# Performance work log

Hardware: AMD Instinct MI355X
Metric: run time of the kernel (lower is better)

Reference implementation:

```python
import jax, jax.numpy as jnp
import numpy as np


def _deform_unfold(feat, offset):
    """Deformable 3x3 unfold with bilinear sampling, zero padding outside.
    feat: [B,C,H,W], offset: [B,2K,H,W] (y,x per point). Returns [B,C,K,H,W]."""
    B, C, H, W = feat.shape
    K = offset.shape[1] // 2
    off = offset.reshape(B, K, 2, H, W)
    # 3x3 kernel grid, dilation 1, padding 1 -> relative taps in {-1,0,1}
    ky = (jnp.arange(K) // 3 - 1).astype(feat.dtype)
    kx = (jnp.arange(K) % 3 - 1).astype(feat.dtype)
    hh = jnp.arange(H, dtype=feat.dtype)
    ww = jnp.arange(W, dtype=feat.dtype)
    py = hh[None, None, :, None] + ky[None, :, None, None] + off[:, :, 0]  # [B,K,H,W]
    px = ww[None, None, None, :] + kx[None, :, None, None] + off[:, :, 1]  # [B,K,H,W]
    y0 = jnp.floor(py)
    x0 = jnp.floor(px)
    fy = py - y0  # frac weights
    fx = px - x0
    y0i = y0.astype(jnp.int32)
    x0i = x0.astype(jnp.int32)

    def gather(yi, xi):
        valid = ((yi >= 0) & (yi < H) & (xi >= 0) & (xi < W)).astype(feat.dtype)
        yc = jnp.clip(yi, 0, H - 1)
        xc = jnp.clip(xi, 0, W - 1)
        v = jax.vmap(lambda f, yy, xx: f[:, yy, xx])(feat, yc, xc)  # [B,C,K,H,W]
        return v * valid[:, None]

    w00 = ((1 - fy) * (1 - fx))[:, None]
    w01 = ((1 - fy) * fx)[:, None]
    w10 = (fy * (1 - fx))[:, None]
    w11 = (fy * fx)[:, None]
    return (gather(y0i, x0i) * w00 + gather(y0i, x0i + 1) * w01 +
            gather(y0i + 1, x0i) * w10 + gather(y0i + 1, x0i + 1) * w11)


def setup_inputs() -> dict:
    key = jax.random.key(0)
    ks = jax.random.split(key, 8)
    B, C, H, W = 4, 256, 64, 64
    Ci, P = 128, 9
    x = jax.random.normal(ks[0], (B, C, H, W), jnp.float32)
    offset = jax.random.normal(ks[1], (B, 2 * P, H, W), jnp.float32)
    std = 0.01  # normal_init(std=0.01)
    Wq = jax.random.normal(ks[2], (Ci, C), jnp.float32) * std
    Wk = jax.random.normal(ks[3], (Ci, C), jnp.float32) * std
    Wv = jax.random.normal(ks[4], (Ci, C), jnp.float32) * std
    Wo = jax.random.normal(ks[5], (Ci,), jnp.float32) * std
    bq = jnp.zeros((Ci,), jnp.float32)
    bk = jnp.zeros((Ci,), jnp.float32)
    bv = jnp.zeros((Ci,), jnp.float32)
    bo = jnp.zeros((1,), jnp.float32)
    return {"x": x, "offset": offset, "Wq": Wq, "bq": bq, "Wk": Wk, "bk": bk,
            "Wv": Wv, "bv": bv, "Wo": Wo, "bo": bo}


def reference(x, offset, Wq, bq, Wk, bk, Wv, bv, Wo, bo):
    # 1x1 conv projections
    q = jnp.einsum('bchw,oc->bohw', x, Wq) + bq[None, :, None, None]
    k = jnp.einsum('bchw,oc->bohw', x, Wk) + bk[None, :, None, None]
    v = jnp.einsum('bchw,oc->bohw', x, Wv) + bv[None, :, None, None]
    qu = _deform_unfold(q, offset)  # [B,Ci,K,H,W]
    ku = _deform_unfold(k, offset)  # [B,Ci,K,H,W]
    vu = _deform_unfold(v, offset)  # [B,Ci,K,H,W]
    # per-pixel KxK attention: query [K,Ci] @ key [Ci,K]
    scores = jnp.einsum('bcihw,bcjhw->bijhw', qu, ku)  # [B,K,K,H,W]
    attn = jax.nn.softmax(scores, axis=2)
    # attn [K,K] @ value [K,Ci]
    out_v = jnp.einsum('bijhw,bcjhw->bcihw', attn, vu)  # [B,Ci,K,H,W]
    # conv_out: 1x1 conv Ci->1 over the value, then sigmoid -> [B,K,H,W]
    out = jnp.einsum('bcihw,c->bihw', out_v, Wo) + bo[0]
    return jax.nn.sigmoid(out)
```

## Files before the change

kernel.cpp:

```cpp
#include <hip/hip_runtime.h>

typedef unsigned short u16;
typedef unsigned int u32;

#define B_   4
#define C_   256
#define CI_  128
#define H_   64
#define W_   64
#define NPB_ 4096
#define NP_  16384
#define K_   9
#define MROWS_ 272

typedef __attribute__((ext_vector_type(8))) __bf16 bf16x8_t;
typedef __attribute__((ext_vector_type(4))) float f32x4_t;
typedef __attribute__((ext_vector_type(2))) float f32x2_t;

__device__ __forceinline__ float bf2f(u16 u) {
    union { u32 i; float f; } x; x.i = ((u32)u) << 16; return x.f;
}
__device__ __forceinline__ float bf2f_lo(u32 w) {
    union { u32 i; float f; } x; x.i = w << 16; return x.f;
}
__device__ __forceinline__ float bf2f_hi(u32 w) {
    union { u32 i; float f; } x; x.i = w & 0xffff0000u; return x.f;
}
__device__ __forceinline__ u16 f2bf(float f) {
    union { float f; u32 i; } x; x.f = f;
    u32 lsb = (x.i >> 16) & 1u;
    return (u16)((x.i + 0x7fffu + lsb) >> 16);
}
__device__ __forceinline__ void acc8p(f32x2_t* f, uint4 v, f32x2_t w2) {
    f32x2_t p;
    p.x = bf2f_lo(v.x); p.y = bf2f_hi(v.x); f[0] += w2 * p;
    p.x = bf2f_lo(v.y); p.y = bf2f_hi(v.y); f[1] += w2 * p;
    p.x = bf2f_lo(v.z); p.y = bf2f_hi(v.z); f[2] += w2 * p;
    p.x = bf2f_lo(v.w); p.y = bf2f_hi(v.w); f[3] += w2 * p;
}

__global__ void k0b_prep(const float* __restrict__ Wq, const float* __restrict__ bq,
                         const float* __restrict__ Wk, const float* __restrict__ bk,
                         const float* __restrict__ Wv, const float* __restrict__ bv,
                         const float* __restrict__ Wo,
                         u16* __restrict__ Wt, float* __restrict__ bias) {
    const int o = blockIdx.x;
    const int c = threadIdx.x;
    u16 val;
    if (o < 128) {
        val = f2bf(Wq[o * C_ + c]);
        if (c == 0) bias[o] = bq[o];
    } else if (o < 256) {
        val = f2bf(Wk[(o - 128) * C_ + c]);
        if (c == 0) bias[o] = bk[o - 128];
    } else if (o == 256) {
        float s = 0.f;
        #pragma unroll 8
        for (int oo = 0; oo < CI_; ++oo)
            s += Wo[oo] * Wv[oo * C_ + c];
        val = f2bf(s);
        if (c == 0) {
            float ts = 0.f;
            #pragma unroll 8
            for (int oo = 0; oo < CI_; ++oo) ts += Wo[oo] * bv[oo];
            bias[256] = ts;
        }
    } else {
        val = 0;
        if (c == 0) bias[o] = 0.f;
    }
    const int mt = o >> 4, l16 = o & 15;
    const int kk = c >> 5, g = (c >> 3) & 3, e = c & 7;
    Wt[(size_t)((mt * 8 + kk) * 64 + g * 16 + l16) * 8 + e] = val;
}

__global__ __launch_bounds__(512) void k1_proj(
    const float* __restrict__ x, const u16* __restrict__ Wt,
    const float* __restrict__ bias,
    u16* __restrict__ qk, float* __restrict__ vs) {
    __shared__ u16 xs[16][272];
    const int t = threadIdx.x;
    const int l = t & 63;
    const int w = t >> 6;
    const int lane16 = l & 15;
    const int g = l >> 4;
    const int p0 = blockIdx.x * 16;
    const int b = p0 >> 12;
    const int pin = p0 & 4095;

    {
        const int spx = t & 15, cg = t >> 4;
        const float* src = x + (size_t)(b * C_ + cg * 8) * NPB_ + pin + spx;
        float v[8];
        #pragma unroll
        for (int i = 0; i < 8; ++i) v[i] = src[(size_t)i * NPB_];
        uint4 pk;
        pk.x = (u32)f2bf(v[0]) | ((u32)f2bf(v[1]) << 16);
        pk.y = (u32)f2bf(v[2]) | ((u32)f2bf(v[3]) << 16);
        pk.z = (u32)f2bf(v[4]) | ((u32)f2bf(v[5]) << 16);
        pk.w = (u32)f2bf(v[6]) | ((u32)f2bf(v[7]) << 16);
        *reinterpret_cast<uint4*>(&xs[spx][cg * 8]) = pk;
    }
    __syncthreads();

    const int mts[3] = {2 * w, 2 * w + 1, 16};
    f32x4_t acc[3];
    #pragma unroll
    for (int n = 0; n < 3; ++n)
        #pragma unroll
        for (int r = 0; r < 4; ++r)
            acc[n][r] = bias[mts[n] * 16 + g * 4 + r];

    #pragma unroll
    for (int kk = 0; kk < 8; ++kk) {
        const bf16x8_t bv = *reinterpret_cast<const bf16x8_t*>(&xs[lane16][kk * 32 + g * 8]);
        #pragma unroll
        for (int n = 0; n < 3; ++n) {
            const bf16x8_t av = *reinterpret_cast<const bf16x8_t*>(
                Wt + (size_t)((mts[n] * 8 + kk) * 64 + l) * 8);
            acc[n] = __builtin_amdgcn_mfma_f32_16x16x32_bf16(av, bv, acc[n], 0, 0, 0);
        }
    }

    const int px = p0 + lane16;
    u16* qrow = qk + (size_t)px * C_;
    #pragma unroll
    for (int n = 0; n < 2; ++n) {
        const int mt = mts[n];
        u32* dst = reinterpret_cast<u32*>(qrow + mt * 16 + g * 4);
        dst[0] = (u32)f2bf(acc[n][0]) | ((u32)f2bf(acc[n][1]) << 16);
        dst[1] = (u32)f2bf(acc[n][2]) | ((u32)f2bf(acc[n][3]) << 16);
    }
    if (w == 0 && g == 0) vs[px] = acc[2][0];
}

__global__ __launch_bounds__(256, 1) void k2_attn(
    const float* __restrict__ off, const u16* __restrict__ qk,
    const float* __restrict__ vs, const float* __restrict__ bo,
    float* __restrict__ out) {
    const int t = threadIdx.x;
    const int l = t & 63;
    const int bid = blockIdx.x;
    const int swz = (bid & 7) * ((int)gridDim.x >> 3) + (bid >> 3);
    const int pixel = swz * 4 + (t >> 6);
    const int b = pixel >> 12;
    const int rem = pixel & 4095;
    const int y = rem >> 6, xx = rem & 63;
    const int l16 = l & 15;
    const int tap = (l16 < K_) ? l16 : (K_ - 1);
    const int g = l >> 4;

    const float* offb = off + ((size_t)b * (2 * K_) + 2 * tap) * NPB_ + rem;
    const float oy = offb[0];
    const float ox = offb[NPB_];
    const float py = (float)(y + tap / 3 - 1) + oy;
    const float px = (float)(xx + tap % 3 - 1) + ox;
    const float fy0 = floorf(py), fx0 = floorf(px);
    const float fy = py - fy0, fx = px - fx0;
    const int y0 = (int)fy0, x0 = (int)fx0;

    const u16* qkb = qk + ((size_t)(b << 12)) * C_ + g * 8;
    const float* vsm = vs + (b << 12);

    float wgt[4];
    int ppc[4];
    const u16* bp[4];
    #pragma unroll
    for (int c = 0; c < 4; ++c) {
        const int dy = c >> 1, dx = c & 1;
        const int yi = y0 + dy, xi = x0 + dx;
        const float wv = (dy ? fy : 1.f - fy) * (dx ? fx : 1.f - fx);
        const int ok = (yi >= 0) & (yi < H_) & (xi >= 0) & (xi < W_);
        const int yc = min(max(yi, 0), H_ - 1);
        const int xc = min(max(xi, 0), W_ - 1);
        ppc[c] = yc * W_ + xc;
        wgt[c] = ok ? wv : 0.f;
        bp[c] = qkb + (size_t)ppc[c] * C_;
    }

    uint4 qv[4][4], kv[4][4];
    #pragma unroll
    for (int c = 0; c < 4; ++c) {
        #pragma unroll
        for (int s = 0; s < 4; ++s) {
            qv[c][s] = *reinterpret_cast<const uint4*>(bp[c] + s * 32);
            kv[c][s] = *reinterpret_cast<const uint4*>(bp[c] + CI_ + s * 32);
        }
    }
    float vsc[4];
    #pragma unroll
    for (int c = 0; c < 4; ++c) vsc[c] = vsm[ppc[c]];
    __builtin_amdgcn_sched_barrier(0);

    const float vsu_t = wgt[0] * vsc[0] + wgt[1] * vsc[1] +
                        wgt[2] * vsc[2] + wgt[3] * vsc[3];

    f32x2_t fq[16], fk[16];
    #pragma unroll
    for (int e = 0; e < 16; ++e) { fq[e] = (f32x2_t){0.f, 0.f}; fk[e] = (f32x2_t){0.f, 0.f}; }
    #pragma unroll
    for (int s = 0; s < 4; ++s) {
        #pragma unroll
        for (int c = 0; c < 4; ++c) {
            const f32x2_t w2 = {wgt[c], wgt[c]};
            acc8p(&fq[s * 4], qv[c][s], w2);
            acc8p(&fk[s * 4], kv[c][s], w2);
        }
    }

    f32x4_t acc = {0.f, 0.f, 0.f, 0.f};
    #pragma unroll
    for (int s = 0; s < 4; ++s) {
        bf16x8_t av, bv;
        #pragma unroll
        for (int e = 0; e < 4; ++e) {
            av[2 * e]     = (__bf16)fk[s * 4 + e].x;
            av[2 * e + 1] = (__bf16)fk[s * 4 + e].y;
            bv[2 * e]     = (__bf16)fq[s * 4 + e].x;
            bv[2 * e + 1] = (__bf16)fq[s * 4 + e].y;
        }
        acc = __builtin_amdgcn_mfma_f32_16x16x32_bf16(av, bv, acc, 0, 0, 0);
    }

    float mx = -1e30f;
    #pragma unroll
    for (int r = 0; r < 4; ++r) {
        const int j = g * 4 + r;
        if (j < K_) mx = fmaxf(mx, acc[r]);
    }
    mx = fmaxf(mx, __shfl_xor(mx, 16, 64));
    mx = fmaxf(mx, __shfl_xor(mx, 32, 64));

    float vj[4];
    #pragma unroll
    for (int r = 0; r < 4; ++r) vj[r] = __shfl(vsu_t, g * 4 + r, 64);

    float den = 0.f, num = 0.f;
    #pragma unroll
    for (int r = 0; r < 4; ++r) {
        const int j = g * 4 + r;
        if (j < K_) {
            const float e = __expf(acc[r] - mx);
            den += e;
            num += e * vj[r];
        }
    }
    den += __shfl_xor(den, 16, 64); den += __shfl_xor(den, 32, 64);
    num += __shfl_xor(num, 16, 64); num += __shfl_xor(num, 32, 64);

    if (l < K_) {
        const float z = num / den + bo[0];
        out[(size_t)b * K_ * NPB_ + (size_t)l * NPB_ + rem] = 1.f / (1.f + __expf(-z));
    }
}

extern "C" void kernel_launch(void* const* d_in, const int* in_sizes, int n_in,
                              void* d_out, int out_size, void* d_ws, size_t ws_size,
                              hipStream_t stream) {
    const float* x   = (const float*)d_in[0];
    const float* off = (const float*)d_in[1];
    const float* Wq  = (const float*)d_in[2];
    const float* bq  = (const float*)d_in[3];
    const float* Wk  = (const float*)d_in[4];
    const float* bk  = (const float*)d_in[5];
    const float* Wv  = (const float*)d_in[6];
    const float* bv  = (const float*)d_in[7];
    const float* Wo  = (const float*)d_in[8];
    const float* bo  = (const float*)d_in[9];
    float* out = (float*)d_out;

    char* ws = (char*)d_ws;
    u16*   qkbuf = (u16*)(ws + 4096);
    float* vsmap = (float*)(ws + 4096 + 8388608);
    u16*   Wt    = (u16*)(ws + 4096 + 8388608 + 65536);
    float* bias  = (float*)(ws + 4096 + 8388608 + 65536 + 139264);

    k0b_prep<<<MROWS_, 256, 0, stream>>>(Wq, bq, Wk, bk, Wv, bv, Wo, Wt, bias);
    k1_proj<<<NP_ / 16, 512, 0, stream>>>(x, Wt, bias, qkbuf, vsmap);
    k2_attn<<<NP_ / 4, 256, 0, stream>>>(off, qkbuf, vsmap, bo, out);
}
```

Before: 76.93 us.

## Compute attention on raw corner rows via MFMA, apply bilinear weights afterwards

The attention kernel no longer interpolates q/k rows in fp32 and then repacks them to bf16. Each lane now loads one bilinear corner row for up to three taps and feeds the raw bf16 rows straight into a 3x3 grid of MFMAs. The bilinear weights are applied to the 16x16 corner-pair score tiles afterwards using shuffles. This removes the conversion and FMA work and the large register footprint, and the 1-wave-per-SIMD launch bound is dropped to allow higher occupancy. In exchange it issues nine times as many MFMAs plus many cross-lane shuffles, and rounding differs because q/k are no longer re-quantised after interpolation.

Result: no change. 77.93 us (median of 2 runs) (+1.3%).

```diff
diff --git a/kernel.cpp b/kernel.cpp
--- a/kernel.cpp
+++ b/kernel.cpp
@@ -15,28 +15,11 @@
 
 typedef __attribute__((ext_vector_type(8))) __bf16 bf16x8_t;
 typedef __attribute__((ext_vector_type(4))) float f32x4_t;
-typedef __attribute__((ext_vector_type(2))) float f32x2_t;
-
-__device__ __forceinline__ float bf2f(u16 u) {
-    union { u32 i; float f; } x; x.i = ((u32)u) << 16; return x.f;
-}
-__device__ __forceinline__ float bf2f_lo(u32 w) {
-    union { u32 i; float f; } x; x.i = w << 16; return x.f;
-}
-__device__ __forceinline__ float bf2f_hi(u32 w) {
-    union { u32 i; float f; } x; x.i = w & 0xffff0000u; return x.f;
-}
+
 __device__ __forceinline__ u16 f2bf(float f) {
     union { float f; u32 i; } x; x.f = f;
     u32 lsb = (x.i >> 16) & 1u;
     return (u16)((x.i + 0x7fffu + lsb) >> 16);
-}
-__device__ __forceinline__ void acc8p(f32x2_t* f, uint4 v, f32x2_t w2) {
-    f32x2_t p;
-    p.x = bf2f_lo(v.x); p.y = bf2f_hi(v.x); f[0] += w2 * p;
-    p.x = bf2f_lo(v.y); p.y = bf2f_hi(v.y); f[1] += w2 * p;
-    p.x = bf2f_lo(v.z); p.y = bf2f_hi(v.z); f[2] += w2 * p;
-    p.x = bf2f_lo(v.w); p.y = bf2f_hi(v.w); f[3] += w2 * p;
 }
 
 __global__ void k0b_prep(const float* __restrict__ Wq, const float* __restrict__ bq,
@@ -134,7 +117,7 @@
     if (w == 0 && g == 0) vs[px] = acc[2][0];
 }
 
-__global__ __launch_bounds__(256, 1) void k2_attn(
+__global__ __launch_bounds__(256) void k2_attn(
     const float* __restrict__ off, const u16* __restrict__ qk,
     const float* __restrict__ vs, const float* __restrict__ bo,
     float* __restrict__ out) {
@@ -146,111 +129,126 @@
     const int b = pixel >> 12;
     const int rem = pixel & 4095;
     const int y = rem >> 6, xx = rem & 63;
-    const int l16 = l & 15;
-    const int tap = (l16 < K_) ? l16 : (K_ - 1);
-    const int g = l >> 4;
-
-    const float* offb = off + ((size_t)b * (2 * K_) + 2 * tap) * NPB_ + rem;
-    const float oy = offb[0];
-    const float ox = offb[NPB_];
-    const float py = (float)(y + tap / 3 - 1) + oy;
-    const float px = (float)(xx + tap % 3 - 1) + ox;
-    const float fy0 = floorf(py), fx0 = floorf(px);
-    const float fy = py - fy0, fx = px - fx0;
-    const int y0 = (int)fy0, x0 = (int)fx0;
-
-    const u16* qkb = qk + ((size_t)(b << 12)) * C_ + g * 8;
+    const int lo = l & 15;
+    const int hi = l >> 4;
+    const int csub = lo >> 2;
+    const int cnr = lo & 3;
+
     const float* vsm = vs + (b << 12);
-
-    float wgt[4];
-    int ppc[4];
-    const u16* bp[4];
-    #pragma unroll
-    for (int c = 0; c < 4; ++c) {
-        const int dy = c >> 1, dx = c & 1;
-        const int yi = y0 + dy, xi = x0 + dx;
+    const u16* qkb = qk + ((size_t)(b << 12)) * C_;
+
+    float w[3]; float vsuc[3]; const u16* rowp[3];
+    #pragma unroll
+    for (int tt = 0; tt < 3; ++tt) {
+        int tap = tt * 4 + csub;
+        const int tv = (tap < K_);
+        if (!tv) tap = K_ - 1;
+        const float* offb = off + ((size_t)b * (2 * K_) + 2 * tap) * NPB_ + rem;
+        const float oy = offb[0];
+        const float ox = offb[NPB_];
+        const float py = (float)(y + tap / 3 - 1) + oy;
+        const float px = (float)(xx + tap % 3 - 1) + ox;
+        const float fy0 = floorf(py), fx0 = floorf(px);
+        const float fy = py - fy0, fx = px - fx0;
+        const int dy = cnr >> 1, dx = cnr & 1;
+        const int yi = (int)fy0 + dy, xi = (int)fx0 + dx;
         const float wv = (dy ? fy : 1.f - fy) * (dx ? fx : 1.f - fx);
-        const int ok = (yi >= 0) & (yi < H_) & (xi >= 0) & (xi < W_);
+        const int ok = (yi >= 0) & (yi < H_) & (xi >= 0) & (xi < W_) & tv;
         const int yc = min(max(yi, 0), H_ - 1);
         const int xc = min(max(xi, 0), W_ - 1);
-        ppc[c] = yc * W_ + xc;
-        wgt[c] = ok ? wv : 0.f;
-        bp[c] = qkb + (size_t)ppc[c] * C_;
-    }
-
-    uint4 qv[4][4], kv[4][4];
-    #pragma unroll
-    for (int c = 0; c < 4; ++c) {
-        #pragma unroll
-        for (int s = 0; s < 4; ++s) {
-            qv[c][s] = *reinterpret_cast<const uint4*>(bp[c] + s * 32);
-            kv[c][s] = *reinterpret_cast<const uint4*>(bp[c] + CI_ + s * 32);
-        }
-    }
-    float vsc[4];
-    #pragma unroll
-    for (int c = 0; c < 4; ++c) vsc[c] = vsm[ppc[c]];
-    __builtin_amdgcn_sched_barrier(0);
-
-    const float vsu_t = wgt[0] * vsc[0] + wgt[1] * vsc[1] +
-                        wgt[2] * vsc[2] + wgt[3] * vsc[3];
-
-    f32x2_t fq[16], fk[16];
-    #pragma unroll
-    for (int e = 0; e < 16; ++e) { fq[e] = (f32x2_t){0.f, 0.f}; fk[e] = (f32x2_t){0.f, 0.f}; }
+        const int pp = yc * W_ + xc;
+        w[tt] = ok ? wv : 0.f;
+        vsuc[tt] = w[tt] * vsm[pp];
+        rowp[tt] = qkb + (size_t)pp * C_ + hi * 8;
+    }
+    #pragma unroll
+    for (int tt = 0; tt < 3; ++tt) {
+        vsuc[tt] += __shfl_xor(vsuc[tt], 1, 64);
+        vsuc[tt] += __shfl_xor(vsuc[tt], 2, 64);
+    }
+    float wrow[3][4];
+    #pragma unroll
+    for (int ta = 0; ta < 3; ++ta)
+        #pragma unroll
+        for (int r = 0; r < 4; ++r)
+            wrow[ta][r] = __shfl(w[ta], 20 * hi + r, 64);
+    float vsj[3];
+    #pragma unroll
+    for (int ta = 0; ta < 3; ++ta)
+        vsj[ta] = __shfl(vsuc[ta], 20 * hi, 64);
+
+    f32x4_t acc[3][3];
+    #pragma unroll
+    for (int ta = 0; ta < 3; ++ta)
+        #pragma unroll
+        for (int tb = 0; tb < 3; ++tb)
+            acc[ta][tb] = (f32x4_t){0.f, 0.f, 0.f, 0.f};
     #pragma unroll
     for (int s = 0; s < 4; ++s) {
-        #pragma unroll
-        for (int c = 0; c < 4; ++c) {
-            const f32x2_t w2 = {wgt[c], wgt[c]};
-            acc8p(&fq[s * 4], qv[c][s], w2);
-            acc8p(&fk[s * 4], kv[c][s], w2);
-        }
-    }
-
-    f32x4_t acc = {0.f, 0.f, 0.f, 0.f};
-    #pragma unroll
-    for (int s = 0; s < 4; ++s) {
-        bf16x8_t av, bv;
-        #pragma unroll
-        for (int e = 0; e < 4; ++e) {
-            av[2 * e]     = (__bf16)fk[s * 4 + e].x;
-            av[2 * e + 1] = (__bf16)fk[s * 4 + e].y;
-            bv[2 * e]     = (__bf16)fq[s * 4 + e].x;
-            bv[2 * e + 1] = (__bf16)fq[s * 4 + e].y;
-        }
-        acc = __builtin_amdgcn_mfma_f32_16x16x32_bf16(av, bv, acc, 0, 0, 0);
-    }
-
-    float mx = -1e30f;
-    #pragma unroll
-    for (int r = 0; r < 4; ++r) {
-        const int j = g * 4 + r;
-        if (j < K_) mx = fmaxf(mx, acc[r]);
-    }
-    mx = fmaxf(mx, __shfl_xor(mx, 16, 64));
-    mx = fmaxf(mx, __shfl_xor(mx, 32, 64));
-
-    float vj[4];
-    #pragma unroll
-    for (int r = 0; r < 4; ++r) vj[r] = __shfl(vsu_t, g * 4 + r, 64);
-
-    float den = 0.f, num = 0.f;
-    #pragma unroll
-    for (int r = 0; r < 4; ++r) {
-        const int j = g * 4 + r;
-        if (j < K_) {
-            const float e = __expf(acc[r] - mx);
-            den += e;
-            num += e * vj[r];
-        }
-    }
-    den += __shfl_xor(den, 16, 64); den += __shfl_xor(den, 32, 64);
-    num += __shfl_xor(num, 16, 64); num += __shfl_xor(num, 32, 64);
-
-    if (l < K_) {
-        const float z = num / den + bo[0];
-        out[(size_t)b * K_ * NPB_ + (size_t)l * NPB_ + rem] = 1.f / (1.f + __expf(-z));
+        bf16x8_t qf[3], kf[3];
+        #pragma unroll
+        for (int tt = 0; tt < 3; ++tt) {
+            qf[tt] = *reinterpret_cast<const bf16x8_t*>(rowp[tt] + s * 32);
+            kf[tt] = *reinterpret_cast<const bf16x8_t*>(rowp[tt] + CI_ + s * 32);
+        }
+        #pragma unroll
+        for (int ta = 0; ta < 3; ++ta)
+            #pragma unroll
+            for (int tb = 0; tb < 3; ++tb)
+                acc[ta][tb] = __builtin_amdgcn_mfma_f32_16x16x32_bf16(
+                    kf[ta], qf[tb], acc[ta][tb], 0, 0, 0);
+    }
+
+    float Sv[3][3];
+    #pragma unroll
+    for (int ta = 0; ta < 3; ++ta) {
+        #pragma unroll
+        for (int tb = 0; tb < 3; ++tb) {
+            float s0 = 0.f;
+            #pragma unroll
+            for (int r = 0; r < 4; ++r) {
+                float u = acc[ta][tb][r] * w[tb];
+                u += __shfl_xor(u, 1, 64);
+                u += __shfl_xor(u, 2, 64);
+                s0 += wrow[ta][r] * u;
+            }
+            Sv[tb][ta] = s0;
+        }
+    }
+
+    const float bof = bo[0];
+    float outv[3];
+    #pragma unroll
+    for (int tb = 0; tb < 3; ++tb) {
+        float mx = -1e30f;
+        #pragma unroll
+        for (int ta = 0; ta < 3; ++ta)
+            if (ta < 2) mx = fmaxf(mx, Sv[tb][ta]);
+            else if (hi == 0) mx = fmaxf(mx, Sv[tb][ta]);
+        mx = fmaxf(mx, __shfl_xor(mx, 16, 64));
+        mx = fmaxf(mx, __shfl_xor(mx, 32, 64));
+        float den = 0.f, num = 0.f;
+        #pragma unroll
+        for (int ta = 0; ta < 3; ++ta) {
+            if (ta < 2 || hi == 0) {
+                const float e = __expf(Sv[tb][ta] - mx);
+                den += e;
+                num += e * vsj[ta];
+            }
+        }
+        den += __shfl_xor(den, 16, 64); den += __shfl_xor(den, 32, 64);
+        num += __shfl_xor(num, 16, 64); num += __shfl_xor(num, 32, 64);
+        outv[tb] = num / den + bof;
+    }
+
+    if (cnr == 0 && hi == 0) {
+        #pragma unroll
+        for (int tb = 0; tb < 3; ++tb) {
+            const int i = tb * 4 + csub;
+            if (i < K_)
+                out[(size_t)b * K_ * NPB_ + (size_t)i * NPB_ + rem] =
+                    1.f / (1.f + __expf(-outv[tb]));
+        }
     }
 }
 
```
